# Optimization experiments

Measured on AMD Instinct MI355X. Metric: run time of the kernel, lower is better.

The kernel has to match this reference:

```python
import jax, jax.numpy as jnp
import numpy as np

IN_DIM = 64
OUT_DIM = 16  # SPD matrix side
HIDDEN = [128, 128]
CHOL_DIM = OUT_DIM + OUT_DIM * (OUT_DIM - 1) // 2  # 136
BATCH = 65536
LEAKY_SLOPE = 0.01  # torch.nn.LeakyReLU default


def _uniform(key, shape, in_feat):
    b = 1.0 / in_feat
    return jax.random.uniform(key, shape, jnp.float32, -b, b)


def setup_inputs() -> dict:
    key = jax.random.key(0)
    ks = jax.random.split(key, 7)
    x = jax.random.normal(ks[0], (BATCH, IN_DIM), jnp.float32)
    # layer sizes: 64 -> 128 -> 128 -> 136, init uniform(-1/in_feat, 1/in_feat)
    W1 = _uniform(ks[1], (IN_DIM, HIDDEN[0]), IN_DIM)
    b1 = _uniform(ks[2], (HIDDEN[0],), IN_DIM)
    W2 = _uniform(ks[3], (HIDDEN[0], HIDDEN[1]), HIDDEN[0])
    b2 = _uniform(ks[4], (HIDDEN[1],), HIDDEN[0])
    W3 = _uniform(ks[5], (HIDDEN[1], CHOL_DIM), HIDDEN[1])
    b3 = _uniform(ks[6], (CHOL_DIM,), HIDDEN[1])
    return {"x": x, "W1": W1, "b1": b1, "W2": W2, "b2": b2, "W3": W3, "b3": b3}


def reference(x, W1, b1, W2, b2, W3, b3):
    # MLP with LeakyReLU between layers, then Tanh on final output
    h = jax.nn.leaky_relu(x @ W1 + b1, LEAKY_SLOPE)
    h = jax.nn.leaky_relu(h @ W2 + b2, LEAKY_SLOPE)
    ldata = jnp.tanh(h @ W3 + b3)  # [B, 136]

    # fill_tril: scatter the 136 values into the lower triangle (row-major)
    rows, cols = jnp.tril_indices(OUT_DIM)
    L = jnp.zeros((x.shape[0], OUT_DIM, OUT_DIM), x.dtype).at[:, rows, cols].set(ldata)
    Q = L + jnp.swapaxes(L, -1, -2)  # symmetric [B, 16, 16]

    # symmetric eigendecomposition (ascending eigenvalues, like torch.symeig)
    w, V = jnp.linalg.eigh(Q)
    # sqrt(softmax(exp(w)**2)) ; exp(w)**2 == exp(2w)
    ev = jnp.sqrt(jax.nn.softmax(jnp.exp(2.0 * w), axis=-1))  # [B, 16]
    # faithful to source: uses inverse (== V^T in exact math since V orthogonal)
    Vinv = jnp.linalg.inv(V)
    # V @ diag(ev) @ V^{-1}
    return jnp.einsum('bij,bj,bjk->bik', V, ev, Vinv)
```

## Files before the change

### kernel.cpp

```cpp
#include <hip/hip_runtime.h>
#include <math.h>

typedef _Float16 f16;
typedef _Float16 half4_t __attribute__((ext_vector_type(4)));
typedef _Float16 half8_t __attribute__((ext_vector_type(8)));
typedef float floatx4 __attribute__((ext_vector_type(4)));

#define LDATA_OFF_BYTES 86016

__global__ __launch_bounds__(256) void prep_weights(
    const float* __restrict__ W1, const float* __restrict__ W2,
    const float* __restrict__ W3, f16* __restrict__ wt) {
  int t = blockIdx.x * 256 + threadIdx.x;
  if (t < 8192) {
    int c = t >> 6, k = t & 63;
    wt[t] = (f16)W1[k * 128 + c];
  } else if (t < 24576) {
    int u = t - 8192;
    int c = u >> 7, k = u & 127;
    wt[t] = (f16)W2[k * 128 + c];
  } else if (t < 43008) {
    int u = t - 24576;
    int c = u >> 7, k = u & 127;
    wt[t] = (f16)((c < 136) ? W3[k * 136 + c] : 0.0f);
  }
}

__device__ __forceinline__ float fast_tanh(float v) {
  float e = __builtin_amdgcn_exp2f(v * 2.885390081777926814f);
  return 1.0f - 2.0f * __builtin_amdgcn_rcpf(e + 1.0f);
}

__global__ __launch_bounds__(64, 1) void mlp_kernel(
    const float* __restrict__ x, const float* __restrict__ b1,
    const float* __restrict__ b2v, const float* __restrict__ b3,
    const f16* __restrict__ wt, f16* __restrict__ ldata) {
  __shared__ f16 act[2048];
  const int lane = threadIdx.x & 63;
  const int cl = lane & 15;
  const int q = lane >> 4;
  const f16* w1t = wt;
  const f16* w2t = wt + 8192;
  const f16* w3t = wt + 24576;

  half8_t w2f[32], w3f[36];
#pragma unroll
  for (int c8 = 0; c8 < 8; ++c8) {
    int c = c8 * 16 + cl;
#pragma unroll
    for (int ks = 0; ks < 4; ++ks)
      w2f[c8 * 4 + ks] = *(const half8_t*)(w2t + c * 128 + ks * 32 + q * 8);
  }
#pragma unroll
  for (int c8 = 0; c8 < 9; ++c8) {
    int c = c8 * 16 + cl;
#pragma unroll
    for (int ks = 0; ks < 4; ++ks)
      w3f[c8 * 4 + ks] = *(const half8_t*)(w3t + c * 128 + ks * 32 + q * 8);
  }
  float bb1[8], bb2[8], bb3[9];
#pragma unroll
  for (int c8 = 0; c8 < 8; ++c8) {
    bb1[c8] = b1[c8 * 16 + cl];
    bb2[c8] = b2v[c8 * 16 + cl];
    bb3[c8] = b3[c8 * 16 + cl];
  }
  bb3[8] = (cl < 8) ? b3[128 + cl] : 0.f;

  const int tile0 = blockIdx.x * 4;
  const float* xp = x + (size_t)(tile0 * 16 + cl) * 64 + q * 8;
  floatx4 v0 = *(const floatx4*)xp;
  floatx4 v1 = *(const floatx4*)(xp + 4);
  floatx4 v2 = *(const floatx4*)(xp + 32);
  floatx4 v3 = *(const floatx4*)(xp + 36);

  for (int t = 0; t < 4; ++t) {
    const int r0 = (tile0 + t) * 16;
    half8_t a0, a1;
#pragma unroll
    for (int i = 0; i < 4; ++i) {
      a0[i] = (f16)v0[i]; a0[i + 4] = (f16)v1[i];
      a1[i] = (f16)v2[i]; a1[i + 4] = (f16)v3[i];
    }
    if (t < 3) {
      xp = x + (size_t)((tile0 + t + 1) * 16 + cl) * 64 + q * 8;
      v0 = *(const floatx4*)xp;
      v1 = *(const floatx4*)(xp + 4);
      v2 = *(const floatx4*)(xp + 32);
      v3 = *(const floatx4*)(xp + 36);
    }

#pragma unroll
    for (int c8 = 0; c8 < 8; ++c8) {
      int c = c8 * 16 + cl;
      half8_t u0 = *(const half8_t*)(w1t + c * 64 + q * 8);
      half8_t u1 = *(const half8_t*)(w1t + c * 64 + 32 + q * 8);
      floatx4 acc = {0.f, 0.f, 0.f, 0.f};
      acc = __builtin_amdgcn_mfma_f32_16x16x32_f16(a0, u0, acc, 0, 0, 0);
      acc = __builtin_amdgcn_mfma_f32_16x16x32_f16(a1, u1, acc, 0, 0, 0);
#pragma unroll
      for (int i = 0; i < 4; ++i) {
        float v = acc[i] + bb1[c8];
        v = v > 0.f ? v : 0.01f * v;
        int row = q * 4 + i;
        int gs = ((c8 * 2 + (cl >> 3)) ^ row) & 15;
        act[row * 128 + gs * 8 + (cl & 7)] = (f16)v;
      }
    }

    half8_t ha[4];
#pragma unroll
    for (int ks = 0; ks < 4; ++ks)
      ha[ks] = *(const half8_t*)(act + cl * 128 +
                                 ((((ks << 2) | q) ^ (cl & 15)) << 3));

#pragma unroll
    for (int c8 = 0; c8 < 8; ++c8) {
      floatx4 acc = {0.f, 0.f, 0.f, 0.f};
#pragma unroll
      for (int ks = 0; ks < 4; ++ks)
        acc = __builtin_amdgcn_mfma_f32_16x16x32_f16(ha[ks], w2f[c8 * 4 + ks],
                                                     acc, 0, 0, 0);
      int c = c8 * 16 + cl;
#pragma unroll
      for (int i = 0; i < 4; ++i) {
        float v = acc[i] + bb2[c8];
        v = v > 0.f ? v : 0.01f * v;
        int row = q * 4 + i;
        int gs = ((c8 * 2 + (cl >> 3)) ^ row) & 15;
        act[row * 128 + gs * 8 + (cl & 7)] = (f16)v;
      }
    }

#pragma unroll
    for (int ks = 0; ks < 4; ++ks)
      ha[ks] = *(const half8_t*)(act + cl * 128 +
                                 ((((ks << 2) | q) ^ (cl & 15)) << 3));

#pragma unroll
    for (int c8 = 0; c8 < 9; ++c8) {
      floatx4 acc = {0.f, 0.f, 0.f, 0.f};
#pragma unroll
      for (int ks = 0; ks < 4; ++ks)
        acc = __builtin_amdgcn_mfma_f32_16x16x32_f16(ha[ks], w3f[c8 * 4 + ks],
                                                     acc, 0, 0, 0);
      int c = c8 * 16 + cl;
      if (c < 136) {
#pragma unroll
        for (int i = 0; i < 4; ++i)
          ldata[(size_t)(r0 + q * 4 + i) * 136 + c] =
              (f16)fast_tanh(acc[i] + bb3[c8]);
      }
    }
  }
}

template <int CTRL>
__device__ __forceinline__ float dpp_add(float v) {
  int t = __builtin_amdgcn_update_dpp(0, __builtin_bit_cast(int, v), CTRL,
                                      0xf, 0xf, true);
  return v + __builtin_bit_cast(float, t);
}
__device__ __forceinline__ float wsum(float v) {
  v = dpp_add<0x111>(v);
  v = dpp_add<0x112>(v);
  v = dpp_add<0x114>(v);
  v = dpp_add<0x118>(v);
  v = dpp_add<0x142>(v);
  v = dpp_add<0x143>(v);
  return __builtin_bit_cast(
      float, __builtin_amdgcn_readlane(__builtin_bit_cast(int, v), 63));
}

__device__ __forceinline__ half4_t to_h(floatx4 v) {
  auto p0 = __builtin_amdgcn_cvt_pkrtz(v[0], v[1]);
  auto p1 = __builtin_amdgcn_cvt_pkrtz(v[2], v[3]);
  half4_t h;
  h[0] = p0[0]; h[1] = p0[1]; h[2] = p1[0]; h[3] = p1[1];
  return h;
}

__device__ __forceinline__ floatx4 expm_c(floatx4 b, floatx4 I4, float& m) {
  float s2 = wsum(b[0] * b[0] + b[1] * b[1] + b[2] * b[2] + b[3] * b[3]);
  float td = wsum(I4[0] * b[0] + I4[1] * b[1] + I4[2] * b[2] + I4[3] * b[3]);
  m = td * 0.0625f;
  float fr2 = fmaxf(s2 - td * m, 1e-30f);
  int e2 = (int)(__builtin_bit_cast(unsigned, fr2) >> 23) - 127;
  int s = (e2 + 5) >> 1;
  s = s < 0 ? 0 : (s > 12 ? 12 : s);
  s = __builtin_amdgcn_readfirstlane(s);
  float sc = __builtin_bit_cast(float, (unsigned)(127 - s) << 23);
  b = (b - I4 * m) * sc;
  half4_t bh = to_h(b);
  floatx4 zero = {0.f, 0.f, 0.f, 0.f};
  floatx4 a2 = __builtin_amdgcn_mfma_f32_16x16x16f16(bh, bh, zero, 0, 0, 0);
  floatx4 t = I4 * 0.5f + b * (1.f / 6.f) + a2 * (1.f / 24.f);
  floatx4 p = __builtin_amdgcn_mfma_f32_16x16x16f16(to_h(a2), to_h(t), I4 + b,
                                                    0, 0, 0);
  for (int k = 0; k < s; ++k) {
    half4_t ph = to_h(p);
    p = __builtin_amdgcn_mfma_f32_16x16x16f16(ph, ph, zero, 0, 0, 0);
  }
  return p;
}

__global__ __launch_bounds__(256) void expm_kernel(
    const f16* __restrict__ ldata, float* __restrict__ out) {
  const int lane = threadIdx.x & 63;
  const int mat = (int)((blockIdx.x * 256u + threadIdx.x) >> 6);
  const int r = lane & 15, q = lane >> 4;
  const f16* ld = ldata + (size_t)mat * 136;

  floatx4 b, I4;
#pragma unroll
  for (int i = 0; i < 4; ++i) {
    int k = q * 4 + i;
    int hi = r > k ? r : k;
    int lo = r + k - hi;
    float v = (float)ld[hi * (hi + 1) / 2 + lo];
    bool d = (r == k);
    I4[i] = d ? 1.f : 0.f;
    b[i] = d ? 4.f * v : 2.f * v;
  }

  float m1;
  floatx4 p = expm_c(b, I4, m1);
  float fac = __builtin_amdgcn_exp2f(m1 * 1.4426950408889634f - 1.0f);
  float m2;
  p = expm_c(p * fac, I4, m2);

  float n2 = wsum(p[0] * p[0] + p[1] * p[1] + p[2] * p[2] + p[3] * p[3]);
  float inv = __builtin_amdgcn_rsqf(n2);
  floatx4 o = p * inv;
  *(floatx4*)(out + (size_t)mat * 256 + r * 16 + q * 4) = o;
}

extern "C" void kernel_launch(void* const* d_in, const int* in_sizes, int n_in,
                              void* d_out, int out_size, void* d_ws,
                              size_t ws_size, hipStream_t stream) {
  const float* x = (const float*)d_in[0];
  const float* W1 = (const float*)d_in[1];
  const float* b1 = (const float*)d_in[2];
  const float* W2 = (const float*)d_in[3];
  const float* b2 = (const float*)d_in[4];
  const float* W3 = (const float*)d_in[5];
  const float* b3 = (const float*)d_in[6];
  float* out = (float*)d_out;
  f16* wt = (f16*)d_ws;
  f16* ldata = (f16*)((char*)d_ws + LDATA_OFF_BYTES);

  prep_weights<<<168, 256, 0, stream>>>(W1, W2, W3, wt);
  mlp_kernel<<<1024, 64, 0, stream>>>(x, b1, b2, b3, wt, ldata);
  expm_kernel<<<16384, 256, 0, stream>>>(ldata, out);
}
```

Baseline: 132.0 us.

## Fuse MLP and matrix-exponential kernels, keeping per-row data in shared memory

Merges the MLP kernel and the expm/normalize kernel into one kernel. Each 256-thread block computes 32 rows of the MLP, with the four waves splitting output column groups, then builds the 32 Cholesky-data vectors in LDS and runs the matrix-exponential stage from LDS. This removes the global round trip of the intermediate ldata buffer and one kernel launch. In exchange it adds block-level barriers between layers, reduces how many rows each block covers, and the expm phase now loops over 8 matrices per wave.

```diff
diff --git a/kernel.cpp b/kernel.cpp
--- a/kernel.cpp
+++ b/kernel.cpp
@@ -5,8 +5,6 @@
 typedef _Float16 half4_t __attribute__((ext_vector_type(4)));
 typedef _Float16 half8_t __attribute__((ext_vector_type(8)));
 typedef float floatx4 __attribute__((ext_vector_type(4)));
-
-#define LDATA_OFF_BYTES 86016
 
 __global__ __launch_bounds__(256) void prep_weights(
     const float* __restrict__ W1, const float* __restrict__ W2,
@@ -29,130 +27,6 @@
 __device__ __forceinline__ float fast_tanh(float v) {
   float e = __builtin_amdgcn_exp2f(v * 2.885390081777926814f);
   return 1.0f - 2.0f * __builtin_amdgcn_rcpf(e + 1.0f);
-}
-
-__global__ __launch_bounds__(64, 1) void mlp_kernel(
-    const float* __restrict__ x, const float* __restrict__ b1,
-    const float* __restrict__ b2v, const float* __restrict__ b3,
-    const f16* __restrict__ wt, f16* __restrict__ ldata) {
-  __shared__ f16 act[2048];
-  const int lane = threadIdx.x & 63;
-  const int cl = lane & 15;
-  const int q = lane >> 4;
-  const f16* w1t = wt;
-  const f16* w2t = wt + 8192;
-  const f16* w3t = wt + 24576;
-
-  half8_t w2f[32], w3f[36];
-#pragma unroll
-  for (int c8 = 0; c8 < 8; ++c8) {
-    int c = c8 * 16 + cl;
-#pragma unroll
-    for (int ks = 0; ks < 4; ++ks)
-      w2f[c8 * 4 + ks] = *(const half8_t*)(w2t + c * 128 + ks * 32 + q * 8);
-  }
-#pragma unroll
-  for (int c8 = 0; c8 < 9; ++c8) {
-    int c = c8 * 16 + cl;
-#pragma unroll
-    for (int ks = 0; ks < 4; ++ks)
-      w3f[c8 * 4 + ks] = *(const half8_t*)(w3t + c * 128 + ks * 32 + q * 8);
-  }
-  float bb1[8], bb2[8], bb3[9];
-#pragma unroll
-  for (int c8 = 0; c8 < 8; ++c8) {
-    bb1[c8] = b1[c8 * 16 + cl];
-    bb2[c8] = b2v[c8 * 16 + cl];
-    bb3[c8] = b3[c8 * 16 + cl];
-  }
-  bb3[8] = (cl < 8) ? b3[128 + cl] : 0.f;
-
-  const int tile0 = blockIdx.x * 4;
-  const float* xp = x + (size_t)(tile0 * 16 + cl) * 64 + q * 8;
-  floatx4 v0 = *(const floatx4*)xp;
-  floatx4 v1 = *(const floatx4*)(xp + 4);
-  floatx4 v2 = *(const floatx4*)(xp + 32);
-  floatx4 v3 = *(const floatx4*)(xp + 36);
-
-  for (int t = 0; t < 4; ++t) {
-    const int r0 = (tile0 + t) * 16;
-    half8_t a0, a1;
-#pragma unroll
-    for (int i = 0; i < 4; ++i) {
-      a0[i] = (f16)v0[i]; a0[i + 4] = (f16)v1[i];
-      a1[i] = (f16)v2[i]; a1[i + 4] = (f16)v3[i];
-    }
-    if (t < 3) {
-      xp = x + (size_t)((tile0 + t + 1) * 16 + cl) * 64 + q * 8;
-      v0 = *(const floatx4*)xp;
-      v1 = *(const floatx4*)(xp + 4);
-      v2 = *(const floatx4*)(xp + 32);
-      v3 = *(const floatx4*)(xp + 36);
-    }
-
-#pragma unroll
-    for (int c8 = 0; c8 < 8; ++c8) {
-      int c = c8 * 16 + cl;
-      half8_t u0 = *(const half8_t*)(w1t + c * 64 + q * 8);
-      half8_t u1 = *(const half8_t*)(w1t + c * 64 + 32 + q * 8);
-      floatx4 acc = {0.f, 0.f, 0.f, 0.f};
-      acc = __builtin_amdgcn_mfma_f32_16x16x32_f16(a0, u0, acc, 0, 0, 0);
-      acc = __builtin_amdgcn_mfma_f32_16x16x32_f16(a1, u1, acc, 0, 0, 0);
-#pragma unroll
-      for (int i = 0; i < 4; ++i) {
-        float v = acc[i] + bb1[c8];
-        v = v > 0.f ? v : 0.01f * v;
-        int row = q * 4 + i;
-        int gs = ((c8 * 2 + (cl >> 3)) ^ row) & 15;
-        act[row * 128 + gs * 8 + (cl & 7)] = (f16)v;
-      }
-    }
-
-    half8_t ha[4];
-#pragma unroll
-    for (int ks = 0; ks < 4; ++ks)
-      ha[ks] = *(const half8_t*)(act + cl * 128 +
-                                 ((((ks << 2) | q) ^ (cl & 15)) << 3));
-
-#pragma unroll
-    for (int c8 = 0; c8 < 8; ++c8) {
-      floatx4 acc = {0.f, 0.f, 0.f, 0.f};
-#pragma unroll
-      for (int ks = 0; ks < 4; ++ks)
-        acc = __builtin_amdgcn_mfma_f32_16x16x32_f16(ha[ks], w2f[c8 * 4 + ks],
-                                                     acc, 0, 0, 0);
-      int c = c8 * 16 + cl;
-#pragma unroll
-      for (int i = 0; i < 4; ++i) {
-        float v = acc[i] + bb2[c8];
-        v = v > 0.f ? v : 0.01f * v;
-        int row = q * 4 + i;
-        int gs = ((c8 * 2 + (cl >> 3)) ^ row) & 15;
-        act[row * 128 + gs * 8 + (cl & 7)] = (f16)v;
-      }
-    }
-
-#pragma unroll
-    for (int ks = 0; ks < 4; ++ks)
-      ha[ks] = *(const half8_t*)(act + cl * 128 +
-                                 ((((ks << 2) | q) ^ (cl & 15)) << 3));
-
-#pragma unroll
-    for (int c8 = 0; c8 < 9; ++c8) {
-      floatx4 acc = {0.f, 0.f, 0.f, 0.f};
-#pragma unroll
-      for (int ks = 0; ks < 4; ++ks)
-        acc = __builtin_amdgcn_mfma_f32_16x16x32_f16(ha[ks], w3f[c8 * 4 + ks],
-                                                     acc, 0, 0, 0);
-      int c = c8 * 16 + cl;
-      if (c < 136) {
-#pragma unroll
-        for (int i = 0; i < 4; ++i)
-          ldata[(size_t)(r0 + q * 4 + i) * 136 + c] =
-              (f16)fast_tanh(acc[i] + bb3[c8]);
-      }
-    }
-  }
 }
 
 template <int CTRL>
@@ -204,35 +78,168 @@
   return p;
 }
 
-__global__ __launch_bounds__(256) void expm_kernel(
-    const f16* __restrict__ ldata, float* __restrict__ out) {
+__global__ __launch_bounds__(256, 2) void fused_kernel(
+    const float* __restrict__ x, const float* __restrict__ b1,
+    const float* __restrict__ b2v, const float* __restrict__ b3,
+    const f16* __restrict__ wt, float* __restrict__ out) {
+  __shared__ f16 act1[2048];
+  __shared__ f16 act2[2048];
+  __shared__ f16 lds_ld[32 * 144];
+
   const int lane = threadIdx.x & 63;
-  const int mat = (int)((blockIdx.x * 256u + threadIdx.x) >> 6);
-  const int r = lane & 15, q = lane >> 4;
-  const f16* ld = ldata + (size_t)mat * 136;
-
-  floatx4 b, I4;
-#pragma unroll
-  for (int i = 0; i < 4; ++i) {
-    int k = q * 4 + i;
-    int hi = r > k ? r : k;
-    int lo = r + k - hi;
-    float v = (float)ld[hi * (hi + 1) / 2 + lo];
-    bool d = (r == k);
-    I4[i] = d ? 1.f : 0.f;
-    b[i] = d ? 4.f * v : 2.f * v;
-  }
-
-  float m1;
-  floatx4 p = expm_c(b, I4, m1);
-  float fac = __builtin_amdgcn_exp2f(m1 * 1.4426950408889634f - 1.0f);
-  float m2;
-  p = expm_c(p * fac, I4, m2);
-
-  float n2 = wsum(p[0] * p[0] + p[1] * p[1] + p[2] * p[2] + p[3] * p[3]);
-  float inv = __builtin_amdgcn_rsqf(n2);
-  floatx4 o = p * inv;
-  *(floatx4*)(out + (size_t)mat * 256 + r * 16 + q * 4) = o;
+  const int w = threadIdx.x >> 6;
+  const int cl = lane & 15;
+  const int q = lane >> 4;
+  const f16* w1t = wt;
+  const f16* w2t = wt + 8192;
+  const f16* w3t = wt + 24576;
+
+  half8_t w1f[2][2], w2f[2][4], w3f[3][4];
+  float bias1[2], bias2[2], bias3[3];
+#pragma unroll
+  for (int j = 0; j < 2; ++j) {
+    int c8g = w + 4 * j;
+    int c = c8g * 16 + cl;
+#pragma unroll
+    for (int ks = 0; ks < 2; ++ks)
+      w1f[j][ks] = *(const half8_t*)(w1t + c * 64 + ks * 32 + q * 8);
+#pragma unroll
+    for (int ks = 0; ks < 4; ++ks)
+      w2f[j][ks] = *(const half8_t*)(w2t + c * 128 + ks * 32 + q * 8);
+    bias1[j] = b1[c];
+    bias2[j] = b2v[c];
+  }
+#pragma unroll
+  for (int j = 0; j < 3; ++j) {
+    int c8g = w + 4 * j;
+    int c8c = c8g < 9 ? c8g : 8;
+    int c = c8c * 16 + cl;
+#pragma unroll
+    for (int ks = 0; ks < 4; ++ks)
+      w3f[j][ks] = *(const half8_t*)(w3t + c * 128 + ks * 32 + q * 8);
+    int cc = c8g * 16 + cl;
+    bias3[j] = (cc < 136) ? b3[cc] : 0.f;
+  }
+
+  const int r0b = blockIdx.x * 32;
+  const float* xp = x + (size_t)(r0b + cl) * 64 + q * 8;
+  floatx4 v0 = *(const floatx4*)xp;
+  floatx4 v1 = *(const floatx4*)(xp + 4);
+  floatx4 v2 = *(const floatx4*)(xp + 32);
+  floatx4 v3 = *(const floatx4*)(xp + 36);
+
+  for (int t = 0; t < 2; ++t) {
+    half8_t a0, a1;
+#pragma unroll
+    for (int i = 0; i < 4; ++i) {
+      a0[i] = (f16)v0[i]; a0[i + 4] = (f16)v1[i];
+      a1[i] = (f16)v2[i]; a1[i + 4] = (f16)v3[i];
+    }
+    if (t == 0) {
+      xp = x + (size_t)(r0b + 16 + cl) * 64 + q * 8;
+      v0 = *(const floatx4*)xp;
+      v1 = *(const floatx4*)(xp + 4);
+      v2 = *(const floatx4*)(xp + 32);
+      v3 = *(const floatx4*)(xp + 36);
+    }
+
+#pragma unroll
+    for (int j = 0; j < 2; ++j) {
+      int c8g = w + 4 * j;
+      floatx4 acc = {0.f, 0.f, 0.f, 0.f};
+      acc = __builtin_amdgcn_mfma_f32_16x16x32_f16(a0, w1f[j][0], acc, 0, 0, 0);
+      acc = __builtin_amdgcn_mfma_f32_16x16x32_f16(a1, w1f[j][1], acc, 0, 0, 0);
+#pragma unroll
+      for (int i = 0; i < 4; ++i) {
+        float v = acc[i] + bias1[j];
+        v = v > 0.f ? v : 0.01f * v;
+        int row = q * 4 + i;
+        int gs = ((c8g * 2 + (cl >> 3)) ^ row) & 15;
+        act1[row * 128 + gs * 8 + (cl & 7)] = (f16)v;
+      }
+    }
+    __syncthreads();
+
+    half8_t ha[4];
+#pragma unroll
+    for (int ks = 0; ks < 4; ++ks)
+      ha[ks] = *(const half8_t*)(act1 + cl * 128 +
+                                 ((((ks << 2) | q) ^ cl) << 3));
+
+#pragma unroll
+    for (int j = 0; j < 2; ++j) {
+      int c8g = w + 4 * j;
+      floatx4 acc = {0.f, 0.f, 0.f, 0.f};
+#pragma unroll
+      for (int ks = 0; ks < 4; ++ks)
+        acc = __builtin_amdgcn_mfma_f32_16x16x32_f16(ha[ks], w2f[j][ks], acc,
+                                                     0, 0, 0);
+#pragma unroll
+      for (int i = 0; i < 4; ++i) {
+        float v = acc[i] + bias2[j];
+        v = v > 0.f ? v : 0.01f * v;
+        int row = q * 4 + i;
+        int gs = ((c8g * 2 + (cl >> 3)) ^ row) & 15;
+        act2[row * 128 + gs * 8 + (cl & 7)] = (f16)v;
+      }
+    }
+    __syncthreads();
+
+#pragma unroll
+    for (int ks = 0; ks < 4; ++ks)
+      ha[ks] = *(const half8_t*)(act2 + cl * 128 +
+                                 ((((ks << 2) | q) ^ cl) << 3));
+
+#pragma unroll
+    for (int j = 0; j < 3; ++j) {
+      int c8g = w + 4 * j;
+      if (c8g < 9) {
+        floatx4 acc = {0.f, 0.f, 0.f, 0.f};
+#pragma unroll
+        for (int ks = 0; ks < 4; ++ks)
+          acc = __builtin_amdgcn_mfma_f32_16x16x32_f16(ha[ks], w3f[j][ks], acc,
+                                                       0, 0, 0);
+        int c = c8g * 16 + cl;
+#pragma unroll
+        for (int i = 0; i < 4; ++i) {
+          float v = fast_tanh(acc[i] + bias3[j]);
+          lds_ld[(t * 16 + q * 4 + i) * 144 + c] = (f16)v;
+        }
+      }
+    }
+  }
+  __syncthreads();
+
+  const int r = cl;
+#pragma unroll 2
+  for (int jj = 0; jj < 8; ++jj) {
+    int m_loc = w * 8 + jj;
+    const f16* ld = lds_ld + m_loc * 144;
+
+    floatx4 b, I4;
+#pragma unroll
+    for (int i = 0; i < 4; ++i) {
+      int k = q * 4 + i;
+      int hi = r > k ? r : k;
+      int lo = r + k - hi;
+      float v = (float)ld[hi * (hi + 1) / 2 + lo];
+      bool d = (r == k);
+      I4[i] = d ? 1.f : 0.f;
+      b[i] = d ? 4.f * v : 2.f * v;
+    }
+
+    float m1;
+    floatx4 p = expm_c(b, I4, m1);
+    float fac = __builtin_amdgcn_exp2f(m1 * 1.4426950408889634f - 1.0f);
+    float m2;
+    p = expm_c(p * fac, I4, m2);
+
+    float n2 = wsum(p[0] * p[0] + p[1] * p[1] + p[2] * p[2] + p[3] * p[3]);
+    float inv = __builtin_amdgcn_rsqf(n2);
+    floatx4 o = p * inv;
+    size_t mat = (size_t)(r0b + m_loc);
+    *(floatx4*)(out + mat * 256 + r * 16 + q * 4) = o;
+  }
 }
 
 extern "C" void kernel_launch(void* const* d_in, const int* in_sizes, int n_in,
@@ -247,9 +254,7 @@
   const float* b3 = (const float*)d_in[6];
   float* out = (float*)d_out;
   f16* wt = (f16*)d_ws;
-  f16* ldata = (f16*)((char*)d_ws + LDATA_OFF_BYTES);
 
   prep_weights<<<168, 256, 0, stream>>>(W1, W2, W3, wt);
-  mlp_kernel<<<1024, 64, 0, stream>>>(x, b1, b2, b3, wt, ldata);
-  expm_kernel<<<16384, 256, 0, stream>>>(ldata, out);
-}
+  fused_kernel<<<2048, 256, 0, stream>>>(x, b1, b2, b3, wt, out);
+}
```

After: 130.9 us. Within noise of the previous version (-0.8%).
